# Kernel optimization log

Measured on AMD Instinct MI355X. Metric: run time of the kernel, lower is better.

Reference implementation:

```python
import jax, jax.numpy as jnp
import numpy as np

B, D_IN, H, D_OUT = 256, 512, 512, 10
S = 32          # num posterior samples
MAXITER = 10    # fixed CG steps (solve_normaleq_cg_fixed_step_reortho(maxiter=10))
EPS = 1e-12


def mlp(params, x):
    W1, b1, W2, b2 = params
    h = jnp.tanh(x @ W1 + b1)
    return h @ W2 + b2  # [B, D_OUT]


def setup_inputs() -> dict:
    key = jax.random.key(0)
    ks = jax.random.split(key, 8)
    s = lambda k, shape, scale=1.0: jax.random.normal(k, shape, dtype=jnp.float32) * scale
    return {
        "x": s(ks[0], (B, D_IN)),
        "W1": s(ks[1], (D_IN, H), 1.0 / np.sqrt(D_IN)),
        "b1": jnp.zeros((H,), jnp.float32),
        "W2": s(ks[2], (H, D_OUT), 1.0 / np.sqrt(H)),
        "b2": jnp.zeros((D_OUT,), jnp.float32),
        "eps_W1": s(ks[3], (S, D_IN, H)),
        "eps_b1": s(ks[4], (S, H)),
        "eps_W2": s(ks[5], (S, H, D_OUT)),
        "eps_b2": s(ks[6], (S, D_OUT)),
        "log_precision": jnp.zeros((), jnp.float32),
        "log_scale_image": jnp.asarray(-2.0, jnp.float32),
    }


def _posterior_predict(x, W1, b1, W2, b2, eps_W1, eps_b1, eps_W2, eps_b2,
                       log_precision, log_scale_image):
    params = (W1, b1, W2, b2)
    f = lambda p: mlp(p, x)
    out0, jvp_lin = jax.linearize(f, params)  # out0: [B, D_OUT]
    _, vjp_fn = jax.vjp(f, params)
    N = B * D_OUT

    def matvec(u_flat):  # u: [N] -> (J J^T) u : [N]
        (t,) = vjp_fn(u_flat.reshape(B, D_OUT))  # J^T u (param pytree)
        return jvp_lin(t).ravel()                # J J^T u

    def cg_reortho(b):  # fixed-step CG with full reorthogonalization
        rn0 = jnp.linalg.norm(b)
        basis0 = jnp.zeros((MAXITER + 1, N), b.dtype).at[0].set(b / (rn0 + EPS))

        def step(carry, k):
            a, r, p, basis = carry
            Ap = matvec(p)
            rr = jnp.vdot(r, r)
            alpha = rr / (jnp.vdot(p, Ap) + EPS)
            a = a + alpha * p
            r_new = r - alpha * Ap
            # Gram-Schmidt reorthogonalization against stored residual basis
            r_new = r_new - basis.T @ (basis @ r_new)
            beta = jnp.vdot(r_new, r_new) / (rr + EPS)
            p = r_new + beta * p
            basis = basis.at[k + 1].set(r_new / (jnp.linalg.norm(r_new) + EPS))
            return (a, r_new, p, basis), jnp.linalg.norm(r_new)

        init = (jnp.zeros_like(b), b, b, basis0)
        (a, _, _, _), resnorms = jax.lax.scan(step, init, jnp.arange(MAXITER))
        return a, resnorms

    def kernel_projection(eps):  # eps: param-pytree iso noise sample
        b = jvp_lin(eps).ravel()          # J v
        a, resnorms = cg_reortho(b)       # (J J^T)^{-1} J v
        (kv,) = vjp_fn(a.reshape(B, D_OUT))  # kernel component J^T a
        return kv, resnorms

    iso = (eps_W1, eps_b1, eps_W2, eps_b2)  # leading axis S
    kernel, resnorms = jax.vmap(kernel_projection)(iso)
    image = jax.tree_util.tree_map(lambda i, k: i - k, iso, kernel)

    # linearized output sampling: f(mean) + J @ (s_k * kernel + s_i * image)
    sk = jnp.exp(-0.5 * log_precision)  # log_scale_kernel = -0.5 * log_precision
    si = jnp.exp(log_scale_image)
    perturb = jax.tree_util.tree_map(lambda kv, iv: sk * kv + si * iv, kernel, image)
    preds = out0[None] + jax.vmap(jvp_lin)(perturb)  # [S, B, D_OUT]
    return preds


def reference(x, W1, b1, W2, b2, eps_W1, eps_b1, eps_W2, eps_b2,
              log_precision, log_scale_image):
    return _posterior_predict(x, W1, b1, W2, b2, eps_W1, eps_b1, eps_W2,
                              eps_b2, log_precision, log_scale_image)
```

## Files before the change

kernel.cpp:

```cpp
#include <hip/hip_runtime.h>
#include <math.h>

#define BB    256
#define DIN   512
#define HD    512
#define DOUT  10
#define NS    32
#define NIDX  2560
#define MAXIT 10
#define CG_EPS 1e-12f

typedef __attribute__((ext_vector_type(8))) short s16x8;
typedef __attribute__((ext_vector_type(4))) float f32x4;
typedef __attribute__((ext_vector_type(4))) unsigned u32x4;

__device__ __forceinline__ float wave_red(float v){
  #pragma unroll
  for (int off = 32; off > 0; off >>= 1) v += __shfl_down(v, off, 64);
  return v;
}
__device__ __forceinline__ unsigned short f2bf(float f){
  unsigned u = __float_as_uint(f);
  return (unsigned short)((u + 0x7FFFu + ((u >> 16) & 1u)) >> 16);
}
__device__ __forceinline__ float bf2f(unsigned short h){
  return __uint_as_float((unsigned)h << 16);
}
__device__ __forceinline__ unsigned cvt_pk_bf16(float a, float b){
  unsigned r;
  asm("v_cvt_pk_bf16_f32 %0, %1, %2" : "=v"(r) : "v"(a), "v"(b));
  return r;
}

typedef const __attribute__((address_space(1))) unsigned short gus_t;
typedef __attribute__((address_space(3))) unsigned short lus_t;
__device__ __forceinline__ void gload16(const unsigned short* g, unsigned short* l){
  __builtin_amdgcn_global_load_lds((gus_t*)g, (lus_t*)l, 16, 0, 0);
}

__global__ __launch_bounds__(256) void k_gemm_z(
    const float* __restrict__ x, const float* __restrict__ W1,
    const float* __restrict__ b1, float* __restrict__ h, float* __restrict__ G)
{
  __shared__ __align__(16) float Al[16][68];
  __shared__ __align__(16) float Bl[16][64];
  const int tid = threadIdx.x;
  const int m0 = blockIdx.y * 64, n0 = blockIdx.x * 64;
  const int tx = tid & 15, ty = tid >> 4;
  float acc[4][4] = {};
  for (int k0 = 0; k0 < DIN; k0 += 16){
    {
      int m = tid >> 2, kk = (tid & 3) << 2;
      float4 a = *(const float4*)(x + (size_t)(m0+m)*DIN + k0 + kk);
      Al[kk+0][m]=a.x; Al[kk+1][m]=a.y; Al[kk+2][m]=a.z; Al[kk+3][m]=a.w;
    }
    {
      int kk = tid >> 4, n = (tid & 15) << 2;
      *(float4*)&Bl[kk][n] = *(const float4*)(W1 + (size_t)(k0+kk)*HD + n0 + n);
    }
    __syncthreads();
    #pragma unroll
    for (int kk = 0; kk < 16; kk++){
      float4 av = *(const float4*)&Al[kk][ty<<2];
      float4 bv = *(const float4*)&Bl[kk][tx<<2];
      float aa[4]={av.x,av.y,av.z,av.w}, bb[4]={bv.x,bv.y,bv.z,bv.w};
      #pragma unroll
      for (int i=0;i<4;i++)
        #pragma unroll
        for (int j=0;j<4;j++) acc[i][j] += aa[i]*bb[j];
    }
    __syncthreads();
  }
  float4 b4 = *(const float4*)&b1[n0 + (tx<<2)];
  float bbv[4] = {b4.x,b4.y,b4.z,b4.w};
  #pragma unroll
  for (int i=0;i<4;i++){
    int m = m0 + (ty<<2) + i;
    float hh[4], gg[4];
    #pragma unroll
    for (int j=0;j<4;j++){ float t = tanhf(acc[i][j] + bbv[j]); hh[j]=t; gg[j]=1.0f-t*t; }
    *(float4*)&h[(size_t)m*HD + n0 + (tx<<2)] = make_float4(hh[0],hh[1],hh[2],hh[3]);
    *(float4*)&G[(size_t)m*HD + n0 + (tx<<2)] = make_float4(gg[0],gg[1],gg[2],gg[3]);
  }
}

__global__ __launch_bounds__(256) void k_gemm_kxkh(
    const float* __restrict__ x, const float* __restrict__ h,
    float* __restrict__ Kx, float* __restrict__ Kh)
{
  __shared__ __align__(16) float Al[16][68];
  __shared__ __align__(16) float Bl[16][68];
  const int tid = threadIdx.x;
  const float* A = blockIdx.z ? h : x;
  float* C = blockIdx.z ? Kh : Kx;
  const int m0 = blockIdx.y * 64, n0 = blockIdx.x * 64;
  const int tx = tid & 15, ty = tid >> 4;
  float acc[4][4] = {};
  for (int k0 = 0; k0 < DIN; k0 += 16){
    {
      int m = tid >> 2, kk = (tid & 3) << 2;
      float4 a = *(const float4*)(A + (size_t)(m0+m)*DIN + k0 + kk);
      Al[kk+0][m]=a.x; Al[kk+1][m]=a.y; Al[kk+2][m]=a.z; Al[kk+3][m]=a.w;
      float4 b = *(const float4*)(A + (size_t)(n0+m)*DIN + k0 + kk);
      Bl[kk+0][m]=b.x; Bl[kk+1][m]=b.y; Bl[kk+2][m]=b.z; Bl[kk+3][m]=b.w;
    }
    __syncthreads();
    #pragma unroll
    for (int kk = 0; kk < 16; kk++){
      float4 av = *(const float4*)&Al[kk][ty<<2];
      float4 bv = *(const float4*)&Bl[kk][tx<<2];
      float aa[4]={av.x,av.y,av.z,av.w}, bb[4]={bv.x,bv.y,bv.z,bv.w};
      #pragma unroll
      for (int i=0;i<4;i++)
        #pragma unroll
        for (int j=0;j<4;j++) acc[i][j] += aa[i]*bb[j];
    }
    __syncthreads();
  }
  #pragma unroll
  for (int i=0;i<4;i++){
    int m = m0 + (ty<<2) + i;
    *(float4*)&C[(size_t)m*BB + n0 + (tx<<2)] =
        make_float4(acc[i][0]+1.0f, acc[i][1]+1.0f, acc[i][2]+1.0f, acc[i][3]+1.0f);
  }
}

__global__ __launch_bounds__(256) void k_buildEx(
    const float* __restrict__ G, const float* __restrict__ W2,
    const float* __restrict__ x,
    unsigned short* __restrict__ E2, unsigned short* __restrict__ x2)
{
  const int tid = threadIdx.x, bid = blockIdx.x;
  if (bid < 1280){
    int gid = bid * 256 + tid;
    int row = gid >> 7, j4 = (gid & 127) << 2;
    int b = row / 10, o = row - b * 10;
    float4 g = *(const float4*)&G[(size_t)b*HD + j4];
    float e[4] = { g.x * W2[(j4+0)*DOUT + o], g.y * W2[(j4+1)*DOUT + o],
                   g.z * W2[(j4+2)*DOUT + o], g.w * W2[(j4+3)*DOUT + o] };
    unsigned short hi[4], lo[4];
    #pragma unroll
    for (int r = 0; r < 4; r++){
      hi[r] = f2bf(e[r]);
      lo[r] = f2bf(e[r] - bf2f(hi[r]));
    }
    *(ushort4*)&E2[(size_t)row*1024 + j4]       = make_ushort4(hi[0],hi[1],hi[2],hi[3]);
    *(ushort4*)&E2[(size_t)row*1024 + 512 + j4] = make_ushort4(lo[0],lo[1],lo[2],lo[3]);
  } else {
    int gid = (bid - 1280) * 256 + tid;
    int row = gid >> 7, j4 = (gid & 127) << 2;
    float4 v = *(const float4*)&x[(size_t)row*DIN + j4];
    float e[4] = {v.x, v.y, v.z, v.w};
    unsigned short hi[4], lo[4];
    #pragma unroll
    for (int r = 0; r < 4; r++){
      hi[r] = f2bf(e[r]);
      lo[r] = f2bf(e[r] - bf2f(hi[r]));
    }
    *(ushort4*)&x2[(size_t)row*1024 + j4]       = make_ushort4(hi[0],hi[1],hi[2],hi[3]);
    *(ushort4*)&x2[(size_t)row*1024 + 512 + j4] = make_ushort4(lo[0],lo[1],lo[2],lo[3]);
  }
}

__global__ __launch_bounds__(256) void k_gemm_M(
    const unsigned short* __restrict__ E2, const float* __restrict__ Kx,
    const float* __restrict__ Kh, unsigned short* __restrict__ M2)
{
  __shared__ __align__(16) unsigned short As[128*64];
  __shared__ __align__(16) unsigned short Bs[64*64];
  const int tid = threadIdx.x;
  const int w = tid >> 6, l = tid & 63;
  const int ln = l & 15, kq = l >> 4;
  const int m0 = blockIdx.y << 7, n0 = blockIdx.x << 6;

  const int srow = tid >> 3;
  const int scc  = (tid & 7) ^ (srow & 7);
  const unsigned short* gA = E2 + (size_t)(m0 + srow)*1024 + scc*8;
  const unsigned short* gB = E2 + (size_t)(n0 + srow)*1024 + scc*8;
  unsigned short* lA = As + w*512;
  unsigned short* lB = Bs + w*512;

  f32x4 acc[2][4];
  #pragma unroll
  for (int i = 0; i < 2; i++)
    #pragma unroll
    for (int j = 0; j < 4; j++)
      acc[i][j] = (f32x4){0.f, 0.f, 0.f, 0.f};

  const int xs = ln & 7;

  for (int t = 0; t < 24; ++t){
    const int p = t >> 3, k8 = t & 7;
    const int oa = ((p == 2) ? 512 : 0) + (k8 << 6);
    const int ob = ((p == 1) ? 512 : 0) + (k8 << 6);
    #pragma unroll
    for (int c = 0; c < 4; c++)
      gload16(gA + (size_t)c*32*1024 + oa, lA + c*2048);
    #pragma unroll
    for (int c = 0; c < 2; c++)
      gload16(gB + (size_t)c*32*1024 + ob, lB + c*2048);
    __syncthreads();

    #pragma unroll
    for (int kk = 0; kk < 2; kk++){
      const int kc = kq + (kk << 2);
      const int co = (kc ^ xs) << 3;
      s16x8 af[2], bf[4];
      #pragma unroll
      for (int f = 0; f < 2; f++)
        af[f] = *(const s16x8*)(As + ((w<<5) + (f<<4) + ln)*64 + co);
      #pragma unroll
      for (int f = 0; f < 4; f++)
        bf[f] = *(const s16x8*)(Bs + ((f<<4) + ln)*64 + co);
      #pragma unroll
      for (int fi = 0; fi < 2; fi++)
        #pragma unroll
        for (int fj = 0; fj < 4; fj++)
          acc[fi][fj] = __builtin_amdgcn_mfma_f32_16x16x32_bf16(
              af[fi], bf[fj], acc[fi][fj], 0, 0, 0);
    }
    __syncthreads();
  }

  const int mb = m0 + (w << 5);
  int bmv[2][4], omv[2][4], bnv[4], onv[4];
  #pragma unroll
  for (int f = 0; f < 4; f++){
    int n = n0 + f*16 + ln; bnv[f] = n / 10; onv[f] = n - bnv[f]*10;
  }
  #pragma unroll
  for (int f = 0; f < 2; f++)
    #pragma unroll
    for (int r = 0; r < 4; r++){
      int m = mb + f*16 + kq*4 + r;
      bmv[f][r] = m / 10; omv[f][r] = m - bmv[f][r]*10;
    }
  #pragma unroll
  for (int fi = 0; fi < 2; fi++)
    #pragma unroll
    for (int r = 0; r < 4; r++){
      const int m = mb + fi*16 + kq*4 + r;
      float v[4];
      #pragma unroll
      for (int fj = 0; fj < 4; fj++){
        float vv = Kx[(size_t)bmv[fi][r]*BB + bnv[fj]] * acc[fi][fj][r];
        if (omv[fi][r] == onv[fj]) vv += Kh[(size_t)bmv[fi][r]*BB + bnv[fj]];
        v[fj] = vv;
      }
      #pragma unroll
      for (int p2 = 0; p2 < 2; p2++){
        const float v0 = v[2*p2], v1 = v[2*p2+1];
        const unsigned ph = cvt_pk_bf16(v0, v1);
        const float h0 = __uint_as_float(ph << 16);
        const float h1 = __uint_as_float(ph & 0xFFFF0000u);
        const unsigned pl = cvt_pk_bf16(v0 - h0, v1 - h1);
        const int na = n0 + (2*p2)*16 + ln, nb = na + 16;
        M2[(size_t)m*5120 + na]        = (unsigned short)ph;
        M2[(size_t)m*5120 + nb]        = (unsigned short)(ph >> 16);
        M2[(size_t)m*5120 + 2560 + na] = (unsigned short)pl;
        M2[(size_t)m*5120 + 2560 + nb] = (unsigned short)(pl >> 16);
      }
    }
}

__global__ __launch_bounds__(512) void k_gemm_T(
    const unsigned short* __restrict__ x2, const float* __restrict__ eW1,
    const float* __restrict__ eb1, const float* __restrict__ G,
    float* __restrict__ T)
{
  const int tid = threadIdx.x;
  const int w = tid >> 6, l = tid & 63;
  const int ln = l & 15, kq = l >> 4;
  const int n0 = blockIdx.x << 6;
  const int s  = blockIdx.y;
  const float* Wb = eW1 + (size_t)s * DIN * HD;

  const unsigned short* pa[2];
  #pragma unroll
  for (int f = 0; f < 2; f++)
    pa[f] = x2 + (size_t)(16*(2*w + f) + ln) * 1024 + kq * 8;

  f32x4 acc[2][4];
  #pragma unroll
  for (int i = 0; i < 2; i++)
    #pragma unroll
    for (int j = 0; j < 4; j++)
      acc[i][j] = (f32x4){0.f, 0.f, 0.f, 0.f};

  #pragma unroll 2
  for (int k0 = 0; k0 < DIN; k0 += 32){
    float wv[4][8];
    const float* wp = Wb + (size_t)(k0 + kq*8)*HD + n0 + ln;
    #pragma unroll
    for (int i = 0; i < 8; i++)
      #pragma unroll
      for (int f = 0; f < 4; f++)
        wv[f][i] = wp[(size_t)i*HD + 16*f];

    s16x8 ahi[2], alo[2], bhi[4], blo[4];
    #pragma unroll
    for (int f = 0; f < 2; f++){
      ahi[f] = *(const s16x8*)(pa[f] + k0);
      alo[f] = *(const s16x8*)(pa[f] + 512 + k0);
    }
    #pragma unroll
    for (int f = 0; f < 4; f++){
      u32x4 bh, bl;
      #pragma unroll
      for (int i = 0; i < 4; i++){
        const float v0 = wv[f][2*i], v1 = wv[f][2*i+1];
        const unsigned ph = cvt_pk_bf16(v0, v1);
        bh[i] = ph;
        const float h0 = __uint_as_float(ph << 16);
        const float h1 = __uint_as_float(ph & 0xFFFF0000u);
        bl[i] = cvt_pk_bf16(v0 - h0, v1 - h1);
      }
      bhi[f] = __builtin_bit_cast(s16x8, bh);
      blo[f] = __builtin_bit_cast(s16x8, bl);
    }
    #pragma unroll
    for (int fi = 0; fi < 2; fi++)
      #pragma unroll
      for (int fj = 0; fj < 4; fj++){
        acc[fi][fj] = __builtin_amdgcn_mfma_f32_16x16x32_bf16(ahi[fi], bhi[fj], acc[fi][fj], 0,0,0);
        acc[fi][fj] = __builtin_amdgcn_mfma_f32_16x16x32_bf16(ahi[fi], blo[fj], acc[fi][fj], 0,0,0);
        acc[fi][fj] = __builtin_amdgcn_mfma_f32_16x16x32_bf16(alo[fi], bhi[fj], acc[fi][fj], 0,0,0);
      }
  }

  #pragma unroll
  for (int fj = 0; fj < 4; fj++){
    const int n = n0 + 16*fj + ln;
    const float eb = eb1[(size_t)s*HD + n];
    #pragma unroll
    for (int fi = 0; fi < 2; fi++)
      #pragma unroll
      for (int q = 0; q < 4; q++){
        const int m = 16*(2*w + fi) + kq*4 + q;
        T[((size_t)s*BB + m)*HD + n] = (acc[fi][fj][q] + eb) * G[(size_t)m*HD + n];
      }
  }
}

__global__ __launch_bounds__(256) void k_bvec(
    const float* __restrict__ T, const float* __restrict__ W2,
    const float* __restrict__ h, const float* __restrict__ eW2,
    const float* __restrict__ eb2, const float* __restrict__ b2,
    float* __restrict__ bvec, float* __restrict__ out0, float* __restrict__ rr0_part)
{
  __shared__ __align__(16) float W2t[10][516];
  __shared__ __align__(16) float E2t[10][516];
  __shared__ float wl[4];
  const int tid = threadIdx.x, bid = blockIdx.x;
  const int s = bid / 10;
  const int idx = (bid % 10) * 256 + tid;
  const int b = idx / 10, o = idx - b*10;
  const float* e2 = eW2 + (size_t)s * HD * DOUT;
  for (int i = tid; i < HD*DOUT; i += 256){
    int k = i / 10, oo = i - k*10;
    W2t[oo][k] = W2[i];
    E2t[oo][k] = e2[i];
  }
  __syncthreads();
  const float* Tr = T + ((size_t)s*BB + b) * HD;
  const float* hr = h + (size_t)b * HD;
  const bool do0 = (bid < 10);
  float acc = eb2[s*DOUT + o];
  float a0 = 0.f;
  #pragma unroll 4
  for (int k4 = 0; k4 < HD/4; k4++){
    float4 t4 = *(const float4*)(Tr + (k4<<2));
    float4 h4 = *(const float4*)(hr + (k4<<2));
    float4 w4 = *(const float4*)&W2t[o][k4<<2];
    float4 q4 = *(const float4*)&E2t[o][k4<<2];
    acc += t4.x*w4.x + t4.y*w4.y + t4.z*w4.z + t4.w*w4.w
         + h4.x*q4.x + h4.y*q4.y + h4.z*q4.z + h4.w*q4.w;
    if (do0) a0 += h4.x*w4.x + h4.y*w4.y + h4.z*w4.z + h4.w*w4.w;
  }
  bvec[(size_t)s*NIDX + idx] = acc;
  if (do0) out0[idx] = a0 + b2[o];
  float v = wave_red(acc * acc);
  if ((tid & 63) == 0) wl[tid >> 6] = v;
  __syncthreads();
  if (tid == 0) rr0_part[bid] = wl[0]+wl[1]+wl[2]+wl[3];
}

__global__ __launch_bounds__(256) void k_init(
    const float* __restrict__ bvec, const float* __restrict__ rr0_part,
    float* __restrict__ r, float* __restrict__ p, float* __restrict__ a,
    float* __restrict__ basis, float* __restrict__ rr_arr,
    unsigned short* __restrict__ ps2)
{
  int gid = blockIdx.x * 256 + threadIdx.x;
  int s = gid / NIDX, idx = gid - s * NIDX;
  float rr0 = 0.f;
  #pragma unroll
  for (int i = 0; i < 10; i++) rr0 += rr0_part[s*10 + i];
  float bv = bvec[gid];
  r[gid] = bv; p[gid] = bv; a[gid] = 0.f;
  basis[gid] = bv / (sqrtf(rr0) + CG_EPS);
  unsigned short hh = f2bf(bv);
  ps2[(size_t)s*5120 + idx]        = hh;
  ps2[(size_t)s*5120 + 2560 + idx] = f2bf(bv - bf2f(hh));
  if (threadIdx.x == 0) rr_arr[s] = rr0;
}

__global__ __launch_bounds__(256) void k_matvec(
    const unsigned short* __restrict__ M2, const unsigned short* __restrict__ p2,
    float* __restrict__ Ap_part)
{
  __shared__ float red[4][16][33];
  const int tid = threadIdx.x;
  const int w = tid >> 6, l = tid & 63;
  const int ln = l & 15, kq = l >> 4;
  const int R0 = blockIdx.x << 4;
  const int kh = blockIdx.y;
  const int c0 = kh*640 + w*160;

  const unsigned short* a0p = M2 + (size_t)(R0 + ln)*5120 + c0 + kq*8;
  const unsigned short* q0  = p2 + (size_t)ln*5120        + c0 + kq*8;
  const unsigned short* q1  = p2 + (size_t)(16 + ln)*5120 + c0 + kq*8;

  f32x4 acc[2];
  acc[0] = (f32x4){0.f,0.f,0.f,0.f};
  acc[1] = (f32x4){0.f,0.f,0.f,0.f};

  #pragma unroll
  for (int ch = 0; ch < 5; ch++){
    const int o = ch * 32;
    s16x8 bh0 = *(const s16x8*)(q0 + o);
    s16x8 bl0 = *(const s16x8*)(q0 + 2560 + o);
    s16x8 bh1 = *(const s16x8*)(q1 + o);
    s16x8 bl1 = *(const s16x8*)(q1 + 2560 + o);
    s16x8 a0h = *(const s16x8*)(a0p + o);
    s16x8 a0l = *(const s16x8*)(a0p + 2560 + o);
    acc[0] = __builtin_amdgcn_mfma_f32_16x16x32_bf16(a0h, bh0, acc[0], 0,0,0);
    acc[1] = __builtin_amdgcn_mfma_f32_16x16x32_bf16(a0h, bh1, acc[1], 0,0,0);
    acc[0] = __builtin_amdgcn_mfma_f32_16x16x32_bf16(a0h, bl0, acc[0], 0,0,0);
    acc[1] = __builtin_amdgcn_mfma_f32_16x16x32_bf16(a0h, bl1, acc[1], 0,0,0);
    acc[0] = __builtin_amdgcn_mfma_f32_16x16x32_bf16(a0l, bh0, acc[0], 0,0,0);
    acc[1] = __builtin_amdgcn_mfma_f32_16x16x32_bf16(a0l, bh1, acc[1], 0,0,0);
  }

  #pragma unroll
  for (int g = 0; g < 2; g++)
    #pragma unroll
    for (int q = 0; q < 4; q++)
      red[w][kq*4 + q][16*g + ln] = acc[g][q];
  __syncthreads();
  #pragma unroll
  for (int j = 0; j < 2; j++){
    const int idx = tid + (j << 8);
    const int r = idx & 15, s = idx >> 4;
    float v = red[0][r][s] + red[1][r][s] + red[2][r][s] + red[3][r][s];
    Ap_part[((size_t)kh*NS + s)*NIDX + R0 + r] = v;
  }
}

__global__ __launch_bounds__(512) void k_cg(
    const float* __restrict__ Ap_part, float* __restrict__ rr_arr, int k, int last,
    float* __restrict__ pv, unsigned short* __restrict__ ps2,
    unsigned short* __restrict__ as2,
    float* __restrict__ av, float* __restrict__ rv, float* __restrict__ basis)
{
  __shared__ float wl[8];
  __shared__ float red[8][10];
  __shared__ float cbr[10];
  const int s = blockIdx.x, tid = threadIdx.x;
  const int w = tid >> 6;
  const size_t base = (size_t)s * NIDX;
  const float rr = rr_arr[s];

  float ap[5], pvv[5];
  #pragma unroll
  for (int c = 0; c < 5; c++){
    const int idx = tid + (c << 9);
    float apv = 0.f;
    #pragma unroll
    for (int kc = 0; kc < 4; kc++)
      apv += Ap_part[((size_t)kc*NS + s)*NIDX + idx];
    ap[c]  = apv;
    pvv[c] = pv[base + idx];
  }
  float v = 0.f;
  #pragma unroll
  for (int c = 0; c < 5; c++) v += pvv[c] * ap[c];
  v = wave_red(v);
  if ((tid & 63) == 0) wl[w] = v;
  __syncthreads();
  const float pAp = wl[0]+wl[1]+wl[2]+wl[3]+wl[4]+wl[5]+wl[6]+wl[7];
  const float alpha = rr / (pAp + CG_EPS);

  float rn[5];
  #pragma unroll
  for (int c = 0; c < 5; c++){
    const int idx = tid + (c << 9);
    const float an = av[base + idx] + alpha * pvv[c];
    av[base + idx] = an;
    rn[c] = rv[base + idx] - alpha * ap[c];
    if (last){
      unsigned short hh = f2bf(an);
      as2[(size_t)s*5120 + idx]        = hh;
      as2[(size_t)s*5120 + 2560 + idx] = f2bf(an - bf2f(hh));
    }
  }

  for (int j = 0; j <= k; j++){
    float cv = 0.f;
    const float* brow = basis + (size_t)j * (NS*NIDX) + base;
    #pragma unroll
    for (int c = 0; c < 5; c++) cv += brow[tid + (c << 9)] * rn[c];
    cv = wave_red(cv);
    if ((tid & 63) == 0) red[w][j] = cv;
  }
  __syncthreads();
  if (tid <= k){
    float cs = 0.f;
    #pragma unroll
    for (int ww = 0; ww < 8; ww++) cs += red[ww][tid];
    cbr[tid] = cs;
  }
  __syncthreads();

  for (int j = 0; j <= k; j++){
    const float cc = cbr[j];
    const float* brow = basis + (size_t)j * (NS*NIDX) + base;
    #pragma unroll
    for (int c = 0; c < 5; c++) rn[c] -= brow[tid + (c << 9)] * cc;
  }

  float rr2 = 0.f;
  #pragma unroll
  for (int c = 0; c < 5; c++) rr2 += rn[c]*rn[c];
  rr2 = wave_red(rr2);
  __syncthreads();
  if ((tid & 63) == 0) wl[w] = rr2;
  __syncthreads();
  const float rrn = wl[0]+wl[1]+wl[2]+wl[3]+wl[4]+wl[5]+wl[6]+wl[7];
  const float beta = rrn / (rr + CG_EPS);
  const float inv  = 1.0f / (sqrtf(rrn) + CG_EPS);

  float* bnew = basis + (size_t)(k+1) * (NS*NIDX) + base;
  #pragma unroll
  for (int c = 0; c < 5; c++){
    const int idx = tid + (c << 9);
    const float pnew = rn[c] + beta * pvv[c];
    rv[base + idx] = rn[c];
    pv[base + idx] = pnew;
    bnew[idx] = rn[c] * inv;
    unsigned short hh = f2bf(pnew);
    ps2[(size_t)s*5120 + idx]        = hh;
    ps2[(size_t)s*5120 + 2560 + idx] = f2bf(pnew - bf2f(hh));
  }
  if (tid == 0) rr_arr[s] = rrn;
}

__global__ __launch_bounds__(256) void k_final(
    const float* __restrict__ out0, const float* __restrict__ bvec,
    const float* __restrict__ Ap_part, const float* __restrict__ lp,
    const float* __restrict__ lsi, float* __restrict__ out)
{
  int gid = blockIdx.x * 256 + threadIdx.x;
  int s = gid / NIDX, idx = gid - s * NIDX;
  float sk = expf(-0.5f * lp[0]);
  float si = expf(lsi[0]);
  float ma = 0.f;
  #pragma unroll
  for (int kc = 0; kc < 4; kc++) ma += Ap_part[(size_t)kc*NS*NIDX + gid];
  out[gid] = out0[idx] + si * bvec[gid] + (sk - si) * ma;
}

extern "C" void kernel_launch(void* const* d_in, const int* in_sizes, int n_in,
                              void* d_out, int out_size, void* d_ws, size_t ws_size,
                              hipStream_t stream)
{
  const float* x   = (const float*)d_in[0];
  const float* W1  = (const float*)d_in[1];
  const float* b1  = (const float*)d_in[2];
  const float* W2  = (const float*)d_in[3];
  const float* b2  = (const float*)d_in[4];
  const float* eW1 = (const float*)d_in[5];
  const float* eb1 = (const float*)d_in[6];
  const float* eW2 = (const float*)d_in[7];
  const float* eb2 = (const float*)d_in[8];
  const float* lp  = (const float*)d_in[9];
  const float* lsi = (const float*)d_in[10];
  float* outp = (float*)d_out;

  float* ws = (float*)d_ws;
  float* h        = ws;
  float* G        = h        + 131072;
  float* Kx       = G        + 131072;
  float* Kh       = Kx       + 65536;
  float* E2f      = Kh       + 65536;
  float* x2f      = E2f      + 1310720;
  float* M2f      = x2f      + 131072;
  float* out0     = M2f      + 6553600;
  float* bvec     = out0     + 2560;
  float* rv       = bvec     + 81920;
  float* pv       = rv       + 81920;
  float* av       = pv       + 81920;
  float* basis    = av       + 81920;
  float* Ap_part  = basis    + 901120;
  float* ps2f     = Ap_part  + 327680;
  float* as2f     = ps2f     + 81920;
  float* rr0_part = as2f     + 81920;
  float* rr_arr   = rr0_part + 320;

  unsigned short* E2  = (unsigned short*)E2f;
  unsigned short* x2  = (unsigned short*)x2f;
  unsigned short* M2  = (unsigned short*)M2f;
  unsigned short* ps2 = (unsigned short*)ps2f;
  unsigned short* as2 = (unsigned short*)as2f;
  float* T = M2f;

  k_gemm_z   <<<dim3(8,4),   256, 0, stream>>>(x, W1, b1, h, G);
  k_buildEx  <<<1408,        256, 0, stream>>>(G, W2, x, E2, x2);
  k_gemm_kxkh<<<dim3(4,4,2), 256, 0, stream>>>(x, h, Kx, Kh);
  k_gemm_T   <<<dim3(8,32),  512, 0, stream>>>(x2, eW1, eb1, G, T);
  k_bvec     <<<320,         256, 0, stream>>>(T, W2, h, eW2, eb2, b2, bvec, out0, rr0_part);
  k_gemm_M   <<<dim3(40,20), 256, 0, stream>>>(E2, Kx, Kh, M2);
  k_init     <<<320,         256, 0, stream>>>(bvec, rr0_part, rv, pv, av, basis, rr_arr, ps2);

  for (int k = 0; k < MAXIT; k++){
    k_matvec<<<dim3(160,4), 256, 0, stream>>>(M2, ps2, Ap_part);
    k_cg    <<<NS,          512, 0, stream>>>(Ap_part, rr_arr, k, (k == MAXIT-1),
                                              pv, ps2, as2, av, rv, basis);
  }

  k_matvec<<<dim3(160,4), 256, 0, stream>>>(M2, as2, Ap_part);
  k_final <<<320,         256, 0, stream>>>(out0, bvec, Ap_part, lp, lsi, outp);
}
```

Baseline: 374.4 us.

## Fold forward GEMM into MFMA T-GEMM and split-K the Gram kernels

The scalar fp32 forward GEMM (x@W1, tanh) is removed and computed as an extra blockIdx.y slice of the bf16x3 MFMA T GEMM. That slice writes h, G and a split bf16 copy of h. The G multiply moves from the T epilogue into k_bvec, so the T GEMM no longer depends on G. The small Kx/Kh Gram GEMMs are split four ways along K to launch more blocks, with a new combine kernel adding the partials and the +1 term. This shortens the serial kernel chain and raises parallelism, at the cost of two extra launches, more buffer traffic and one more G read in k_bvec.

Result: no change. 368.4 us (-1.6%).

```diff
diff --git a/kernel.cpp b/kernel.cpp
--- a/kernel.cpp
+++ b/kernel.cpp
@@ -38,65 +38,160 @@
   __builtin_amdgcn_global_load_lds((gus_t*)g, (lus_t*)l, 16, 0, 0);
 }
 
-__global__ __launch_bounds__(256) void k_gemm_z(
-    const float* __restrict__ x, const float* __restrict__ W1,
-    const float* __restrict__ b1, float* __restrict__ h, float* __restrict__ G)
-{
-  __shared__ __align__(16) float Al[16][68];
-  __shared__ __align__(16) float Bl[16][64];
+__global__ __launch_bounds__(256) void k_buildx(
+    const float* __restrict__ x, unsigned short* __restrict__ x2)
+{
+  int gid = blockIdx.x * 256 + threadIdx.x;
+  int row = gid >> 7, j4 = (gid & 127) << 2;
+  float4 v = *(const float4*)&x[(size_t)row*DIN + j4];
+  float e[4] = {v.x, v.y, v.z, v.w};
+  unsigned short hi[4], lo[4];
+  #pragma unroll
+  for (int r = 0; r < 4; r++){
+    hi[r] = f2bf(e[r]);
+    lo[r] = f2bf(e[r] - bf2f(hi[r]));
+  }
+  *(ushort4*)&x2[(size_t)row*1024 + j4]       = make_ushort4(hi[0],hi[1],hi[2],hi[3]);
+  *(ushort4*)&x2[(size_t)row*1024 + 512 + j4] = make_ushort4(lo[0],lo[1],lo[2],lo[3]);
+}
+
+__global__ __launch_bounds__(512) void k_gemm_T(
+    const unsigned short* __restrict__ x2, const float* __restrict__ eW1,
+    const float* __restrict__ eb1, const float* __restrict__ W1,
+    const float* __restrict__ b1, float* __restrict__ T,
+    float* __restrict__ h, float* __restrict__ G, unsigned short* __restrict__ h2)
+{
   const int tid = threadIdx.x;
-  const int m0 = blockIdx.y * 64, n0 = blockIdx.x * 64;
-  const int tx = tid & 15, ty = tid >> 4;
-  float acc[4][4] = {};
-  for (int k0 = 0; k0 < DIN; k0 += 16){
-    {
-      int m = tid >> 2, kk = (tid & 3) << 2;
-      float4 a = *(const float4*)(x + (size_t)(m0+m)*DIN + k0 + kk);
-      Al[kk+0][m]=a.x; Al[kk+1][m]=a.y; Al[kk+2][m]=a.z; Al[kk+3][m]=a.w;
-    }
-    {
-      int kk = tid >> 4, n = (tid & 15) << 2;
-      *(float4*)&Bl[kk][n] = *(const float4*)(W1 + (size_t)(k0+kk)*HD + n0 + n);
-    }
-    __syncthreads();
-    #pragma unroll
-    for (int kk = 0; kk < 16; kk++){
-      float4 av = *(const float4*)&Al[kk][ty<<2];
-      float4 bv = *(const float4*)&Bl[kk][tx<<2];
-      float aa[4]={av.x,av.y,av.z,av.w}, bb[4]={bv.x,bv.y,bv.z,bv.w};
-      #pragma unroll
-      for (int i=0;i<4;i++)
+  const int w = tid >> 6, l = tid & 63;
+  const int ln = l & 15, kq = l >> 4;
+  const int n0 = blockIdx.x << 6;
+  const int s  = blockIdx.y;
+  const bool isz = (s == NS);
+  const float* Wb = isz ? W1 : (eW1 + (size_t)s * DIN * HD);
+
+  const unsigned short* pa[2];
+  #pragma unroll
+  for (int f = 0; f < 2; f++)
+    pa[f] = x2 + (size_t)(16*(2*w + f) + ln) * 1024 + kq * 8;
+
+  f32x4 acc[2][4];
+  #pragma unroll
+  for (int i = 0; i < 2; i++)
+    #pragma unroll
+    for (int j = 0; j < 4; j++)
+      acc[i][j] = (f32x4){0.f, 0.f, 0.f, 0.f};
+
+  #pragma unroll 2
+  for (int k0 = 0; k0 < DIN; k0 += 32){
+    float wv[4][8];
+    const float* wp = Wb + (size_t)(k0 + kq*8)*HD + n0 + ln;
+    #pragma unroll
+    for (int i = 0; i < 8; i++)
+      #pragma unroll
+      for (int f = 0; f < 4; f++)
+        wv[f][i] = wp[(size_t)i*HD + 16*f];
+
+    s16x8 ahi[2], alo[2], bhi[4], blo[4];
+    #pragma unroll
+    for (int f = 0; f < 2; f++){
+      ahi[f] = *(const s16x8*)(pa[f] + k0);
+      alo[f] = *(const s16x8*)(pa[f] + 512 + k0);
+    }
+    #pragma unroll
+    for (int f = 0; f < 4; f++){
+      u32x4 bh, bl;
+      #pragma unroll
+      for (int i = 0; i < 4; i++){
+        const float v0 = wv[f][2*i], v1 = wv[f][2*i+1];
+        const unsigned ph = cvt_pk_bf16(v0, v1);
+        bh[i] = ph;
+        const float h0 = __uint_as_float(ph << 16);
+        const float h1 = __uint_as_float(ph & 0xFFFF0000u);
+        bl[i] = cvt_pk_bf16(v0 - h0, v1 - h1);
+      }
+      bhi[f] = __builtin_bit_cast(s16x8, bh);
+      blo[f] = __builtin_bit_cast(s16x8, bl);
+    }
+    #pragma unroll
+    for (int fi = 0; fi < 2; fi++)
+      #pragma unroll
+      for (int fj = 0; fj < 4; fj++){
+        acc[fi][fj] = __builtin_amdgcn_mfma_f32_16x16x32_bf16(ahi[fi], bhi[fj], acc[fi][fj], 0,0,0);
+        acc[fi][fj] = __builtin_amdgcn_mfma_f32_16x16x32_bf16(ahi[fi], blo[fj], acc[fi][fj], 0,0,0);
+        acc[fi][fj] = __builtin_amdgcn_mfma_f32_16x16x32_bf16(alo[fi], bhi[fj], acc[fi][fj], 0,0,0);
+      }
+  }
+
+  if (!isz){
+    #pragma unroll
+    for (int fj = 0; fj < 4; fj++){
+      const int n = n0 + 16*fj + ln;
+      const float eb = eb1[(size_t)s*HD + n];
+      #pragma unroll
+      for (int fi = 0; fi < 2; fi++)
         #pragma unroll
-        for (int j=0;j<4;j++) acc[i][j] += aa[i]*bb[j];
-    }
-    __syncthreads();
-  }
-  float4 b4 = *(const float4*)&b1[n0 + (tx<<2)];
-  float bbv[4] = {b4.x,b4.y,b4.z,b4.w};
-  #pragma unroll
-  for (int i=0;i<4;i++){
-    int m = m0 + (ty<<2) + i;
-    float hh[4], gg[4];
-    #pragma unroll
-    for (int j=0;j<4;j++){ float t = tanhf(acc[i][j] + bbv[j]); hh[j]=t; gg[j]=1.0f-t*t; }
-    *(float4*)&h[(size_t)m*HD + n0 + (tx<<2)] = make_float4(hh[0],hh[1],hh[2],hh[3]);
-    *(float4*)&G[(size_t)m*HD + n0 + (tx<<2)] = make_float4(gg[0],gg[1],gg[2],gg[3]);
-  }
-}
-
-__global__ __launch_bounds__(256) void k_gemm_kxkh(
+        for (int q = 0; q < 4; q++){
+          const int m = 16*(2*w + fi) + kq*4 + q;
+          T[((size_t)s*BB + m)*HD + n] = acc[fi][fj][q] + eb;
+        }
+    }
+  } else {
+    #pragma unroll
+    for (int fj = 0; fj < 4; fj++){
+      const int n = n0 + 16*fj + ln;
+      const float eb = b1[n];
+      #pragma unroll
+      for (int fi = 0; fi < 2; fi++)
+        #pragma unroll
+        for (int q = 0; q < 4; q++){
+          const int m = 16*(2*w + fi) + kq*4 + q;
+          const float t = tanhf(acc[fi][fj][q] + eb);
+          const float g = 1.0f - t*t;
+          h[(size_t)m*HD + n] = t;
+          G[(size_t)m*HD + n] = g;
+          unsigned short hh = f2bf(t);
+          h2[(size_t)m*1024 + n]       = hh;
+          h2[(size_t)m*1024 + 512 + n] = f2bf(t - bf2f(hh));
+        }
+    }
+  }
+}
+
+__global__ __launch_bounds__(256) void k_buildE(
+    const float* __restrict__ G, const float* __restrict__ W2,
+    unsigned short* __restrict__ E2)
+{
+  int gid = blockIdx.x * 256 + threadIdx.x;
+  int row = gid >> 7, j4 = (gid & 127) << 2;
+  int b = row / 10, o = row - b * 10;
+  float4 g = *(const float4*)&G[(size_t)b*HD + j4];
+  float e[4] = { g.x * W2[(j4+0)*DOUT + o], g.y * W2[(j4+1)*DOUT + o],
+                 g.z * W2[(j4+2)*DOUT + o], g.w * W2[(j4+3)*DOUT + o] };
+  unsigned short hi[4], lo[4];
+  #pragma unroll
+  for (int r = 0; r < 4; r++){
+    hi[r] = f2bf(e[r]);
+    lo[r] = f2bf(e[r] - bf2f(hi[r]));
+  }
+  *(ushort4*)&E2[(size_t)row*1024 + j4]       = make_ushort4(hi[0],hi[1],hi[2],hi[3]);
+  *(ushort4*)&E2[(size_t)row*1024 + 512 + j4] = make_ushort4(lo[0],lo[1],lo[2],lo[3]);
+}
+
+__global__ __launch_bounds__(256) void k_kxkh(
     const float* __restrict__ x, const float* __restrict__ h,
-    float* __restrict__ Kx, float* __restrict__ Kh)
+    float* __restrict__ Kp)
 {
   __shared__ __align__(16) float Al[16][68];
   __shared__ __align__(16) float Bl[16][68];
   const int tid = threadIdx.x;
-  const float* A = blockIdx.z ? h : x;
-  float* C = blockIdx.z ? Kh : Kx;
+  const int which = blockIdx.z >> 2, kc = blockIdx.z & 3;
+  const float* A = which ? h : x;
+  float* C = Kp + (size_t)blockIdx.z * 65536;
   const int m0 = blockIdx.y * 64, n0 = blockIdx.x * 64;
   const int tx = tid & 15, ty = tid >> 4;
+  const int kbase = kc << 7;
   float acc[4][4] = {};
-  for (int k0 = 0; k0 < DIN; k0 += 16){
+  for (int k0 = kbase; k0 < kbase + 128; k0 += 16){
     {
       int m = tid >> 2, kk = (tid & 3) << 2;
       float4 a = *(const float4*)(A + (size_t)(m0+m)*DIN + k0 + kk);
@@ -121,45 +216,18 @@
   for (int i=0;i<4;i++){
     int m = m0 + (ty<<2) + i;
     *(float4*)&C[(size_t)m*BB + n0 + (tx<<2)] =
-        make_float4(acc[i][0]+1.0f, acc[i][1]+1.0f, acc[i][2]+1.0f, acc[i][3]+1.0f);
-  }
-}
-
-__global__ __launch_bounds__(256) void k_buildEx(
-    const float* __restrict__ G, const float* __restrict__ W2,
-    const float* __restrict__ x,
-    unsigned short* __restrict__ E2, unsigned short* __restrict__ x2)
-{
-  const int tid = threadIdx.x, bid = blockIdx.x;
-  if (bid < 1280){
-    int gid = bid * 256 + tid;
-    int row = gid >> 7, j4 = (gid & 127) << 2;
-    int b = row / 10, o = row - b * 10;
-    float4 g = *(const float4*)&G[(size_t)b*HD + j4];
-    float e[4] = { g.x * W2[(j4+0)*DOUT + o], g.y * W2[(j4+1)*DOUT + o],
-                   g.z * W2[(j4+2)*DOUT + o], g.w * W2[(j4+3)*DOUT + o] };
-    unsigned short hi[4], lo[4];
-    #pragma unroll
-    for (int r = 0; r < 4; r++){
-      hi[r] = f2bf(e[r]);
-      lo[r] = f2bf(e[r] - bf2f(hi[r]));
-    }
-    *(ushort4*)&E2[(size_t)row*1024 + j4]       = make_ushort4(hi[0],hi[1],hi[2],hi[3]);
-    *(ushort4*)&E2[(size_t)row*1024 + 512 + j4] = make_ushort4(lo[0],lo[1],lo[2],lo[3]);
-  } else {
-    int gid = (bid - 1280) * 256 + tid;
-    int row = gid >> 7, j4 = (gid & 127) << 2;
-    float4 v = *(const float4*)&x[(size_t)row*DIN + j4];
-    float e[4] = {v.x, v.y, v.z, v.w};
-    unsigned short hi[4], lo[4];
-    #pragma unroll
-    for (int r = 0; r < 4; r++){
-      hi[r] = f2bf(e[r]);
-      lo[r] = f2bf(e[r] - bf2f(hi[r]));
-    }
-    *(ushort4*)&x2[(size_t)row*1024 + j4]       = make_ushort4(hi[0],hi[1],hi[2],hi[3]);
-    *(ushort4*)&x2[(size_t)row*1024 + 512 + j4] = make_ushort4(lo[0],lo[1],lo[2],lo[3]);
-  }
+        make_float4(acc[i][0], acc[i][1], acc[i][2], acc[i][3]);
+  }
+}
+
+__global__ __launch_bounds__(256) void k_comb(
+    const float* __restrict__ Kp, float* __restrict__ Kx, float* __restrict__ Kh)
+{
+  int gid = blockIdx.x * 256 + threadIdx.x;
+  int which = gid >> 16, idx = gid & 65535;
+  const float* base = Kp + (size_t)which * 4 * 65536;
+  float v = base[idx] + base[65536 + idx] + base[2*65536 + idx] + base[3*65536 + idx] + 1.0f;
+  (which ? Kh : Kx)[idx] = v;
 }
 
 __global__ __launch_bounds__(256) void k_gemm_M(
@@ -263,89 +331,11 @@
     }
 }
 
-__global__ __launch_bounds__(512) void k_gemm_T(
-    const unsigned short* __restrict__ x2, const float* __restrict__ eW1,
-    const float* __restrict__ eb1, const float* __restrict__ G,
-    float* __restrict__ T)
-{
-  const int tid = threadIdx.x;
-  const int w = tid >> 6, l = tid & 63;
-  const int ln = l & 15, kq = l >> 4;
-  const int n0 = blockIdx.x << 6;
-  const int s  = blockIdx.y;
-  const float* Wb = eW1 + (size_t)s * DIN * HD;
-
-  const unsigned short* pa[2];
-  #pragma unroll
-  for (int f = 0; f < 2; f++)
-    pa[f] = x2 + (size_t)(16*(2*w + f) + ln) * 1024 + kq * 8;
-
-  f32x4 acc[2][4];
-  #pragma unroll
-  for (int i = 0; i < 2; i++)
-    #pragma unroll
-    for (int j = 0; j < 4; j++)
-      acc[i][j] = (f32x4){0.f, 0.f, 0.f, 0.f};
-
-  #pragma unroll 2
-  for (int k0 = 0; k0 < DIN; k0 += 32){
-    float wv[4][8];
-    const float* wp = Wb + (size_t)(k0 + kq*8)*HD + n0 + ln;
-    #pragma unroll
-    for (int i = 0; i < 8; i++)
-      #pragma unroll
-      for (int f = 0; f < 4; f++)
-        wv[f][i] = wp[(size_t)i*HD + 16*f];
-
-    s16x8 ahi[2], alo[2], bhi[4], blo[4];
-    #pragma unroll
-    for (int f = 0; f < 2; f++){
-      ahi[f] = *(const s16x8*)(pa[f] + k0);
-      alo[f] = *(const s16x8*)(pa[f] + 512 + k0);
-    }
-    #pragma unroll
-    for (int f = 0; f < 4; f++){
-      u32x4 bh, bl;
-      #pragma unroll
-      for (int i = 0; i < 4; i++){
-        const float v0 = wv[f][2*i], v1 = wv[f][2*i+1];
-        const unsigned ph = cvt_pk_bf16(v0, v1);
-        bh[i] = ph;
-        const float h0 = __uint_as_float(ph << 16);
-        const float h1 = __uint_as_float(ph & 0xFFFF0000u);
-        bl[i] = cvt_pk_bf16(v0 - h0, v1 - h1);
-      }
-      bhi[f] = __builtin_bit_cast(s16x8, bh);
-      blo[f] = __builtin_bit_cast(s16x8, bl);
-    }
-    #pragma unroll
-    for (int fi = 0; fi < 2; fi++)
-      #pragma unroll
-      for (int fj = 0; fj < 4; fj++){
-        acc[fi][fj] = __builtin_amdgcn_mfma_f32_16x16x32_bf16(ahi[fi], bhi[fj], acc[fi][fj], 0,0,0);
-        acc[fi][fj] = __builtin_amdgcn_mfma_f32_16x16x32_bf16(ahi[fi], blo[fj], acc[fi][fj], 0,0,0);
-        acc[fi][fj] = __builtin_amdgcn_mfma_f32_16x16x32_bf16(alo[fi], bhi[fj], acc[fi][fj], 0,0,0);
-      }
-  }
-
-  #pragma unroll
-  for (int fj = 0; fj < 4; fj++){
-    const int n = n0 + 16*fj + ln;
-    const float eb = eb1[(size_t)s*HD + n];
-    #pragma unroll
-    for (int fi = 0; fi < 2; fi++)
-      #pragma unroll
-      for (int q = 0; q < 4; q++){
-        const int m = 16*(2*w + fi) + kq*4 + q;
-        T[((size_t)s*BB + m)*HD + n] = (acc[fi][fj][q] + eb) * G[(size_t)m*HD + n];
-      }
-  }
-}
-
 __global__ __launch_bounds__(256) void k_bvec(
     const float* __restrict__ T, const float* __restrict__ W2,
-    const float* __restrict__ h, const float* __restrict__ eW2,
-    const float* __restrict__ eb2, const float* __restrict__ b2,
+    const float* __restrict__ h, const float* __restrict__ G,
+    const float* __restrict__ eW2, const float* __restrict__ eb2,
+    const float* __restrict__ b2,
     float* __restrict__ bvec, float* __restrict__ out0, float* __restrict__ rr0_part)
 {
   __shared__ __align__(16) float W2t[10][516];
@@ -364,6 +354,7 @@
   __syncthreads();
   const float* Tr = T + ((size_t)s*BB + b) * HD;
   const float* hr = h + (size_t)b * HD;
+  const float* Gr = G + (size_t)b * HD;
   const bool do0 = (bid < 10);
   float acc = eb2[s*DOUT + o];
   float a0 = 0.f;
@@ -371,9 +362,10 @@
   for (int k4 = 0; k4 < HD/4; k4++){
     float4 t4 = *(const float4*)(Tr + (k4<<2));
     float4 h4 = *(const float4*)(hr + (k4<<2));
+    float4 g4 = *(const float4*)(Gr + (k4<<2));
     float4 w4 = *(const float4*)&W2t[o][k4<<2];
     float4 q4 = *(const float4*)&E2t[o][k4<<2];
-    acc += t4.x*w4.x + t4.y*w4.y + t4.z*w4.z + t4.w*w4.w
+    acc += t4.x*g4.x*w4.x + t4.y*g4.y*w4.y + t4.z*g4.z*w4.z + t4.w*g4.w*w4.w
          + h4.x*q4.x + h4.y*q4.y + h4.z*q4.z + h4.w*q4.w;
     if (do0) a0 += h4.x*w4.x + h4.y*w4.y + h4.z*w4.z + h4.w*w4.w;
   }
@@ -612,15 +604,18 @@
   unsigned short* M2  = (unsigned short*)M2f;
   unsigned short* ps2 = (unsigned short*)ps2f;
   unsigned short* as2 = (unsigned short*)as2f;
-  float* T = M2f;
-
-  k_gemm_z   <<<dim3(8,4),   256, 0, stream>>>(x, W1, b1, h, G);
-  k_buildEx  <<<1408,        256, 0, stream>>>(G, W2, x, E2, x2);
-  k_gemm_kxkh<<<dim3(4,4,2), 256, 0, stream>>>(x, h, Kx, Kh);
-  k_gemm_T   <<<dim3(8,32),  512, 0, stream>>>(x2, eW1, eb1, G, T);
-  k_bvec     <<<320,         256, 0, stream>>>(T, W2, h, eW2, eb2, b2, bvec, out0, rr0_part);
-  k_gemm_M   <<<dim3(40,20), 256, 0, stream>>>(E2, Kx, Kh, M2);
-  k_init     <<<320,         256, 0, stream>>>(bvec, rr0_part, rv, pv, av, basis, rr_arr, ps2);
+  float* T  = M2f;
+  float* Kp = basis;
+  unsigned short* h2 = (unsigned short*)Ap_part;
+
+  k_buildx <<<128,          256, 0, stream>>>(x, x2);
+  k_gemm_T <<<dim3(8,33),   512, 0, stream>>>(x2, eW1, eb1, W1, b1, T, h, G, h2);
+  k_buildE <<<1280,         256, 0, stream>>>(G, W2, E2);
+  k_kxkh   <<<dim3(4,4,8),  256, 0, stream>>>(x, h, Kp);
+  k_comb   <<<512,          256, 0, stream>>>(Kp, Kx, Kh);
+  k_bvec   <<<320,          256, 0, stream>>>(T, W2, h, G, eW2, eb2, b2, bvec, out0, rr0_part);
+  k_gemm_M <<<dim3(40,20),  256, 0, stream>>>(E2, Kx, Kh, M2);
+  k_init   <<<320,          256, 0, stream>>>(bvec, rr0_part, rv, pv, av, basis, rr_arr, ps2);
 
   for (int k = 0; k < MAXIT; k++){
     k_matvec<<<dim3(160,4), 256, 0, stream>>>(M2, ps2, Ap_part);
```
